# Optimization experiments

Measured on AMD Instinct MI355X. Metric: run time of the kernel, lower is better.

## Reference

```python
import jax, jax.numpy as jnp
import numpy as np

N, E, D, H = 50000, 800000, 64, 8
DH = D // H
EPS = 1e-5


def _bn(x, gamma, beta):
    # BatchNorm1d in training mode: biased variance over the node axis
    m = x.mean(axis=0)
    v = ((x - m) ** 2).mean(axis=0)
    return (x - m) * jax.lax.rsqrt(v + EPS) * gamma + beta


def setup_inputs() -> dict:
    key = jax.random.key(0)
    ks = jax.random.split(key, 12)
    s_in = 1.0 / np.sqrt(D)
    s_ff = 1.0 / np.sqrt(2 * D)
    inp = {
        "h": jax.random.normal(ks[0], (N, D), dtype=jnp.float32),
        "src": jax.random.randint(ks[1], (E,), 0, N, dtype=jnp.int32),
        "dst": jax.random.randint(ks[2], (E,), 0, N, dtype=jnp.int32),
        "Wq": jax.random.normal(ks[3], (D, D), dtype=jnp.float32) * s_in,
        "bq": jnp.zeros((D,), jnp.float32),
        "Wk": jax.random.normal(ks[4], (D, D), dtype=jnp.float32) * s_in,
        "bk": jnp.zeros((D,), jnp.float32),
        "Wv": jax.random.normal(ks[5], (D, D), dtype=jnp.float32) * s_in,
        "bv": jnp.zeros((D,), jnp.float32),
        "g1": jnp.ones((D,), jnp.float32),
        "b1": jnp.zeros((D,), jnp.float32),
        "W1": jax.random.normal(ks[6], (D, 2 * D), dtype=jnp.float32) * s_in,
        "bb1": jnp.zeros((2 * D,), jnp.float32),
        "W2": jax.random.normal(ks[7], (2 * D, D), dtype=jnp.float32) * s_ff,
        "bb2": jnp.zeros((D,), jnp.float32),
        "g2": jnp.ones((D,), jnp.float32),
        "b2": jnp.zeros((D,), jnp.float32),
    }
    return inp


def reference(h, src, dst, Wq, bq, Wk, bk, Wv, bv, g1, b1, W1, bb1, W2, bb2, g2, b2):
    scale = np.sqrt(DH).astype(np.float32)
    Q = (h @ Wq + bq).reshape(N, H, DH)
    K = (h @ Wk + bk).reshape(N, H, DH)
    V = (h @ Wv + bv).reshape(N, H, DH)

    # per-edge score: K[src] . Q[dst], clamped/scaled exp  -> [E, H]
    score = jnp.sum(K[src] * Q[dst], axis=-1)
    score = jnp.exp(jnp.clip(score / scale, -5.0, 5.0))

    # weighted-value and normalizer scatter-sums onto dst nodes
    wV = jax.ops.segment_sum(V[src] * score[:, :, None], dst, num_segments=N)  # [N,H,DH]
    z = jax.ops.segment_sum(score, dst, num_segments=N)  # [N,H]

    safe_z = jnp.where(z == 0, 1.0, z)
    head = jnp.where((z == 0)[:, :, None], 0.0, wV / safe_z[:, :, None])  # nan -> 0
    attn = head.reshape(N, D)

    h1 = _bn(h + attn, g1, b1)
    ffn = jax.nn.relu(h1 @ W1 + bb1) @ W2 + bb2
    out = _bn(h1 + ffn, g2, b2)
    return out
```

## Files before the change

### kernel.cpp

```cpp
#include <hip/hip_runtime.h>
#include <hip/hip_fp16.h>
#include <math.h>

#define N_NODES 50000
#define E_EDGES 800000
#define EPS_BN  1e-5f
#define INV_N   (1.0f / N_NODES)
#define SCAN_BLOCKS 196
#define QKV_BLOCKS  782
#define HIST_BLOCKS 3125

__global__ __launch_bounds__(256) void qkv_hist_kernel(
    const float* __restrict__ h,
    const float* __restrict__ Wq, const float* __restrict__ bq,
    const float* __restrict__ Wk, const float* __restrict__ bk,
    const float* __restrict__ Wv, const float* __restrict__ bv,
    float* __restrict__ Q, __half* __restrict__ KV,
    const int* __restrict__ dst, int* __restrict__ count)
{
    __shared__ float  xs[64][68];
    __shared__ __half Wqh[64][64];
    __shared__ __half Wkh[64][64];
    __shared__ __half Wvh[64][64];
    const int t = threadIdx.x;

    if (blockIdx.x >= QKV_BLOCKS) {
        const int e = (blockIdx.x - QKV_BLOCKS) * 256 + t;
        if (e < E_EDGES) atomicAdd(&count[dst[e]], 1);
        return;
    }

    const int tx = t & 15;
    const int ty = t >> 4;
    const int row0 = blockIdx.x * 64;

    {
        __half2* wq = (__half2*)&Wqh[0][0];
        __half2* wk = (__half2*)&Wkh[0][0];
        __half2* wv = (__half2*)&Wvh[0][0];
        #pragma unroll
        for (int k = 0; k < 4; ++k) {
            const int i = t + k * 256;
            const float4 a = *(const float4*)(Wq + i * 4);
            wq[i * 2]     = __floats2half2_rn(a.x, a.y);
            wq[i * 2 + 1] = __floats2half2_rn(a.z, a.w);
            const float4 b = *(const float4*)(Wk + i * 4);
            wk[i * 2]     = __floats2half2_rn(b.x, b.y);
            wk[i * 2 + 1] = __floats2half2_rn(b.z, b.w);
            const float4 c = *(const float4*)(Wv + i * 4);
            wv[i * 2]     = __floats2half2_rn(c.x, c.y);
            wv[i * 2 + 1] = __floats2half2_rn(c.z, c.w);
        }
    }

    #pragma unroll
    for (int k = 0; k < 4; ++k) {
        const int i  = t + k * 256;
        const int r  = i >> 4;
        const int c4 = (i & 15) * 4;
        float4 v = make_float4(0.f, 0.f, 0.f, 0.f);
        if (row0 + r < N_NODES)
            v = *(const float4*)(h + (size_t)(row0 + r) * 64 + c4);
        *(float4*)(&xs[r][c4]) = v;
    }
    __syncthreads();

    const int c0 = tx * 4;
    float4 aq[4], ak[4], av[4];
    const float4 bq4 = *(const float4*)(bq + c0);
    const float4 bk4 = *(const float4*)(bk + c0);
    const float4 bv4 = *(const float4*)(bv + c0);
    #pragma unroll
    for (int i = 0; i < 4; ++i) { aq[i] = bq4; ak[i] = bk4; av[i] = bv4; }

    #pragma unroll 4
    for (int c = 0; c < 64; ++c) {
        const __half2* qp = (const __half2*)&Wqh[c][c0];
        const __half2* kp = (const __half2*)&Wkh[c][c0];
        const __half2* vp = (const __half2*)&Wvh[c][c0];
        const float2 wq0 = __half22float2(qp[0]);
        const float2 wq1 = __half22float2(qp[1]);
        const float2 wk0 = __half22float2(kp[0]);
        const float2 wk1 = __half22float2(kp[1]);
        const float2 wv0 = __half22float2(vp[0]);
        const float2 wv1 = __half22float2(vp[1]);
        #pragma unroll
        for (int i = 0; i < 4; ++i) {
            const float xv = xs[ty * 4 + i][c];
            aq[i].x = fmaf(xv, wq0.x, aq[i].x); aq[i].y = fmaf(xv, wq0.y, aq[i].y);
            aq[i].z = fmaf(xv, wq1.x, aq[i].z); aq[i].w = fmaf(xv, wq1.y, aq[i].w);
            ak[i].x = fmaf(xv, wk0.x, ak[i].x); ak[i].y = fmaf(xv, wk0.y, ak[i].y);
            ak[i].z = fmaf(xv, wk1.x, ak[i].z); ak[i].w = fmaf(xv, wk1.y, ak[i].w);
            av[i].x = fmaf(xv, wv0.x, av[i].x); av[i].y = fmaf(xv, wv0.y, av[i].y);
            av[i].z = fmaf(xv, wv1.x, av[i].z); av[i].w = fmaf(xv, wv1.y, av[i].w);
        }
    }
    #pragma unroll
    for (int i = 0; i < 4; ++i) {
        const int row = row0 + ty * 4 + i;
        if (row < N_NODES) {
            *(float4*)(Q + (size_t)row * 64 + c0) = aq[i];
            __half* kvp = KV + ((size_t)(c0 >> 3) * N_NODES + row) * 16 + (c0 & 7);
            *(__half2*)(kvp)         = __floats2half2_rn(ak[i].x, ak[i].y);
            *(__half2*)(kvp + 2)     = __floats2half2_rn(ak[i].z, ak[i].w);
            *(__half2*)(kvp + 8)     = __floats2half2_rn(av[i].x, av[i].y);
            *(__half2*)(kvp + 8 + 2) = __floats2half2_rn(av[i].z, av[i].w);
        }
    }
}

__global__ __launch_bounds__(256) void scanA_kernel(
    const int* __restrict__ count,
    int* __restrict__ rowStart, int* __restrict__ blockSums)
{
    __shared__ int ls[256];
    const int t = threadIdx.x;
    const int i = blockIdx.x * 256 + t;
    const int v = (i < N_NODES) ? count[i] : 0;
    ls[t] = v;
    __syncthreads();
    #pragma unroll
    for (int off = 1; off < 256; off <<= 1) {
        const int u = (t >= off) ? ls[t - off] : 0;
        __syncthreads();
        ls[t] += u;
        __syncthreads();
    }
    if (i < N_NODES) rowStart[i] = ls[t] - v;
    if (t == 255) blockSums[blockIdx.x] = ls[255];
}

__global__ __launch_bounds__(256) void scanBC_kernel(
    int* __restrict__ rowStart, int* __restrict__ cursor,
    const int* __restrict__ blockSums)
{
    __shared__ int ls[256];
    const int t = threadIdx.x;
    const int v = (t < SCAN_BLOCKS) ? blockSums[t] : 0;
    ls[t] = v;
    __syncthreads();
    #pragma unroll
    for (int off = 1; off < 256; off <<= 1) {
        const int u = (t >= off) ? ls[t - off] : 0;
        __syncthreads();
        ls[t] += u;
        __syncthreads();
    }
    const int exc = ls[t] - v;
    __syncthreads();
    ls[t] = exc;
    __syncthreads();
    const int boff = ls[blockIdx.x];
    const int i = blockIdx.x * 256 + t;
    if (i < N_NODES) {
        const int r = rowStart[i] + boff;
        rowStart[i] = r;
        cursor[i]   = r;
    }
    if (i == 0) rowStart[N_NODES] = E_EDGES;
}

__global__ __launch_bounds__(256) void scatter_kernel(
    const int* __restrict__ src, const int* __restrict__ dst,
    int* __restrict__ cursor, unsigned short* __restrict__ srcSorted)
{
    const int e0 = blockIdx.x * 512 + threadIdx.x;
    const int e1 = e0 + 256;
    const bool h0 = e0 < E_EDGES;
    const bool h1 = e1 < E_EDGES;
    const int s0 = h0 ? src[e0] : 0;
    const int d0 = h0 ? dst[e0] : 0;
    const int s1 = h1 ? src[e1] : 0;
    const int d1 = h1 ? dst[e1] : 0;
    if (h0) srcSorted[atomicAdd(&cursor[d0], 1)] = (unsigned short)s0;
    if (h1) srcSorted[atomicAdd(&cursor[d1], 1)] = (unsigned short)s1;
}

__global__ __launch_bounds__(256) void gather_edge_kernel(
    const float* __restrict__ h,
    const float* __restrict__ Q, const __half* __restrict__ KV,
    const int* __restrict__ rowStart, const unsigned short* __restrict__ srcSorted,
    float* __restrict__ x, float* __restrict__ s1, float* __restrict__ sq1)
{
    const int lane = threadIdx.x & 63;
    const int wave = threadIdx.x >> 6;
    const int slot = lane & 7;
    const int ns   = lane >> 3;
    const int hh   = blockIdx.x & 7;
    const int chunk0  = blockIdx.x >> 3;
    const int nChunks = gridDim.x >> 3;
    const __half* __restrict__ KVh = KV + (size_t)hh * N_NODES * 16;

    float bsum[8], bsq[8];
    #pragma unroll
    for (int j = 0; j < 8; ++j) { bsum[j] = 0.0f; bsq[j] = 0.0f; }

    for (int chunk = chunk0; chunk * 32 < N_NODES; chunk += nChunks) {
        const int n = chunk * 32 + wave * 8 + ns;
        const bool valid = (n < N_NODES);
        int start = 0, end = 0;
        float4 q0 = make_float4(0.f, 0.f, 0.f, 0.f), q1 = q0;
        if (valid) {
            start = rowStart[n];
            end   = rowStart[n + 1];
            q0 = *(const float4*)(Q + (size_t)n * 64 + hh * 8);
            q1 = *(const float4*)(Q + (size_t)n * 64 + hh * 8 + 4);
        }
        float a0=0,a1=0,a2=0,a3=0,a4=0,a5=0,a6=0,a7=0,zacc=0;
        for (int e = start + slot; e < end; e += 16) {
            const int s0 = srcSorted[e];
            const int e1 = e + 8;
            const bool has1 = (e1 < end);
            const int s1i = has1 ? (int)srcSorted[e1] : s0;
            const __half* kv0 = KVh + (size_t)s0 * 16;
            const __half* kv1 = KVh + (size_t)s1i * 16;
            const float4 kraw0 = *(const float4*)(kv0);
            const float4 vraw0 = *(const float4*)(kv0 + 8);
            const float4 kraw1 = *(const float4*)(kv1);
            const float4 vraw1 = *(const float4*)(kv1 + 8);

            {
                const __half2* kh = (const __half2*)&kraw0;
                const float2 ka = __half22float2(kh[0]);
                const float2 kb = __half22float2(kh[1]);
                const float2 kc = __half22float2(kh[2]);
                const float2 kd = __half22float2(kh[3]);
                float sc = ka.x*q0.x + ka.y*q0.y + kb.x*q0.z + kb.y*q0.w
                         + kc.x*q1.x + kc.y*q1.y + kd.x*q1.z + kd.y*q1.w;
                sc *= 0.35355339059327373f;
                sc = fminf(5.0f, fmaxf(-5.0f, sc));
                const float p = __expf(sc);
                const __half2* vh = (const __half2*)&vraw0;
                const float2 va = __half22float2(vh[0]);
                const float2 vb = __half22float2(vh[1]);
                const float2 vc = __half22float2(vh[2]);
                const float2 vd = __half22float2(vh[3]);
                a0 = fmaf(p, va.x, a0); a1 = fmaf(p, va.y, a1);
                a2 = fmaf(p, vb.x, a2); a3 = fmaf(p, vb.y, a3);
                a4 = fmaf(p, vc.x, a4); a5 = fmaf(p, vc.y, a5);
                a6 = fmaf(p, vd.x, a6); a7 = fmaf(p, vd.y, a7);
                zacc += p;
            }
            if (has1) {
                const __half2* kh = (const __half2*)&kraw1;
                const float2 ka = __half22float2(kh[0]);
                const float2 kb = __half22float2(kh[1]);
                const float2 kc = __half22float2(kh[2]);
                const float2 kd = __half22float2(kh[3]);
                float sc = ka.x*q0.x + ka.y*q0.y + kb.x*q0.z + kb.y*q0.w
                         + kc.x*q1.x + kc.y*q1.y + kd.x*q1.z + kd.y*q1.w;
                sc *= 0.35355339059327373f;
                sc = fminf(5.0f, fmaxf(-5.0f, sc));
                const float p = __expf(sc);
                const __half2* vh = (const __half2*)&vraw1;
                const float2 va = __half22float2(vh[0]);
                const float2 vb = __half22float2(vh[1]);
                const float2 vc = __half22float2(vh[2]);
                const float2 vd = __half22float2(vh[3]);
                a0 = fmaf(p, va.x, a0); a1 = fmaf(p, va.y, a1);
                a2 = fmaf(p, vb.x, a2); a3 = fmaf(p, vb.y, a3);
                a4 = fmaf(p, vc.x, a4); a5 = fmaf(p, vc.y, a5);
                a6 = fmaf(p, vd.x, a6); a7 = fmaf(p, vd.y, a7);
                zacc += p;
            }
        }
        #pragma unroll
        for (int m = 1; m < 8; m <<= 1) {
            a0 += __shfl_xor(a0, m, 64); a1 += __shfl_xor(a1, m, 64);
            a2 += __shfl_xor(a2, m, 64); a3 += __shfl_xor(a3, m, 64);
            a4 += __shfl_xor(a4, m, 64); a5 += __shfl_xor(a5, m, 64);
            a6 += __shfl_xor(a6, m, 64); a7 += __shfl_xor(a7, m, 64);
            zacc += __shfl_xor(zacc, m, 64);
        }
        if (slot == 0 && valid) {
            const float inv = (zacc == 0.0f) ? 0.0f : 1.0f / zacc;
            const float4 h0 = *(const float4*)(h + (size_t)n * 64 + hh * 8);
            const float4 h1 = *(const float4*)(h + (size_t)n * 64 + hh * 8 + 4);
            float xv[8];
            xv[0] = fmaf(a0, inv, h0.x); xv[1] = fmaf(a1, inv, h0.y);
            xv[2] = fmaf(a2, inv, h0.z); xv[3] = fmaf(a3, inv, h0.w);
            xv[4] = fmaf(a4, inv, h1.x); xv[5] = fmaf(a5, inv, h1.y);
            xv[6] = fmaf(a6, inv, h1.z); xv[7] = fmaf(a7, inv, h1.w);
            *(float4*)(x + (size_t)n * 64 + hh * 8)     =
                make_float4(xv[0], xv[1], xv[2], xv[3]);
            *(float4*)(x + (size_t)n * 64 + hh * 8 + 4) =
                make_float4(xv[4], xv[5], xv[6], xv[7]);
            #pragma unroll
            for (int j = 0; j < 8; ++j) {
                bsum[j] += xv[j];
                bsq[j]  += xv[j] * xv[j];
            }
        }
    }
    __shared__ float lsm[32][8];
    __shared__ float lsq[32][8];
    if (slot == 0) {
        #pragma unroll
        for (int j = 0; j < 8; ++j) {
            lsm[wave * 8 + ns][j] = bsum[j];
            lsq[wave * 8 + ns][j] = bsq[j];
        }
    }
    __syncthreads();
    if (threadIdx.x < 8) {
        const int tt = threadIdx.x;
        float ss = 0.f, qq = 0.f;
        #pragma unroll
        for (int k = 0; k < 32; ++k) { ss += lsm[k][tt]; qq += lsq[k][tt]; }
        atomicAdd(s1 + hh * 8 + tt, ss);
        atomicAdd(sq1 + hh * 8 + tt, qq);
    }
}

__global__ __launch_bounds__(512, 4) void ffn_kernel(
    const float* __restrict__ x,
    const float* __restrict__ s1, const float* __restrict__ sq1,
    const float* __restrict__ g1, const float* __restrict__ b1,
    const float* __restrict__ W1, const float* __restrict__ bb1,
    const float* __restrict__ W2, const float* __restrict__ bb2,
    float* __restrict__ y, float* __restrict__ s2, float* __restrict__ sq2)
{
    __shared__ __half W1h[64][128];
    __shared__ __half W2h[128][64];
    __shared__ float  xs[64][64];
    __shared__ __half ts[64][128];

    const int t  = threadIdx.x;
    const int tx = t & 15;
    const int ty = t >> 4;
    const int row0 = blockIdx.x * 64;

    {
        __half2* w1p = (__half2*)&W1h[0][0];
        __half2* w2p = (__half2*)&W2h[0][0];
        #pragma unroll
        for (int k = 0; k < 4; ++k) {
            const int i = t + k * 512;
            const float4 w1 = *(const float4*)(W1 + i * 4);
            w1p[i * 2]     = __floats2half2_rn(w1.x, w1.y);
            w1p[i * 2 + 1] = __floats2half2_rn(w1.z, w1.w);
            const float4 w2 = *(const float4*)(W2 + i * 4);
            w2p[i * 2]     = __floats2half2_rn(w2.x, w2.y);
            w2p[i * 2 + 1] = __floats2half2_rn(w2.z, w2.w);
        }
    }

    {
        const int c4 = tx * 4;
        const float4 ssum = *(const float4*)(s1 + c4);
        const float4 sqs  = *(const float4*)(sq1 + c4);
        const float4 gg   = *(const float4*)(g1 + c4);
        const float4 bb   = *(const float4*)(b1 + c4);
        float4 mm, rr, A, C;
        mm.x = ssum.x * INV_N; mm.y = ssum.y * INV_N;
        mm.z = ssum.z * INV_N; mm.w = ssum.w * INV_N;
        rr.x = rsqrtf(sqs.x * INV_N - mm.x * mm.x + EPS_BN);
        rr.y = rsqrtf(sqs.y * INV_N - mm.y * mm.y + EPS_BN);
        rr.z = rsqrtf(sqs.z * INV_N - mm.z * mm.z + EPS_BN);
        rr.w = rsqrtf(sqs.w * INV_N - mm.w * mm.w + EPS_BN);
        A.x = rr.x * gg.x; C.x = bb.x - mm.x * A.x;
        A.y = rr.y * gg.y; C.y = bb.y - mm.y * A.y;
        A.z = rr.z * gg.z; C.z = bb.z - mm.z * A.z;
        A.w = rr.w * gg.w; C.w = bb.w - mm.w * A.w;
        #pragma unroll
        for (int k = 0; k < 2; ++k) {
            const int i = t + k * 512;
            const int r = i >> 4;
            float4 v = make_float4(0.f, 0.f, 0.f, 0.f);
            if (row0 + r < N_NODES) {
                const float4 xv = *(const float4*)(x + (size_t)(row0 + r) * 64 + c4);
                v.x = fmaf(xv.x, A.x, C.x);
                v.y = fmaf(xv.y, A.y, C.y);
                v.z = fmaf(xv.z, A.z, C.z);
                v.w = fmaf(xv.w, A.w, C.w);
            }
            *(float4*)(&xs[r][c4]) = v;
        }
    }
    __syncthreads();

    const int r0 = ty * 2, r1 = r0 + 1;

    {
        const int cA = tx * 4, cB = 64 + tx * 4;
        float4 aA0 = make_float4(0,0,0,0), aA1 = aA0, aB0 = aA0, aB1 = aA0;
        #pragma unroll 4
        for (int c = 0; c < 64; ++c) {
            const __half2* wAp = (const __half2*)&W1h[c][cA];
            const __half2* wBp = (const __half2*)&W1h[c][cB];
            const float2 wa0 = __half22float2(wAp[0]);
            const float2 wa1 = __half22float2(wAp[1]);
            const float2 wb0 = __half22float2(wBp[0]);
            const float2 wb1 = __half22float2(wBp[1]);
            const float x0 = xs[r0][c];
            const float x1 = xs[r1][c];
            aA0.x = fmaf(x0, wa0.x, aA0.x); aA0.y = fmaf(x0, wa0.y, aA0.y);
            aA0.z = fmaf(x0, wa1.x, aA0.z); aA0.w = fmaf(x0, wa1.y, aA0.w);
            aA1.x = fmaf(x1, wa0.x, aA1.x); aA1.y = fmaf(x1, wa0.y, aA1.y);
            aA1.z = fmaf(x1, wa1.x, aA1.z); aA1.w = fmaf(x1, wa1.y, aA1.w);
            aB0.x = fmaf(x0, wb0.x, aB0.x); aB0.y = fmaf(x0, wb0.y, aB0.y);
            aB0.z = fmaf(x0, wb1.x, aB0.z); aB0.w = fmaf(x0, wb1.y, aB0.w);
            aB1.x = fmaf(x1, wb0.x, aB1.x); aB1.y = fmaf(x1, wb0.y, aB1.y);
            aB1.z = fmaf(x1, wb1.x, aB1.z); aB1.w = fmaf(x1, wb1.y, aB1.w);
        }
        const float4 b1A = *(const float4*)(bb1 + cA);
        const float4 b1B = *(const float4*)(bb1 + cB);
        aA0.x = fmaxf(aA0.x + b1A.x, 0.f); aA0.y = fmaxf(aA0.y + b1A.y, 0.f);
        aA0.z = fmaxf(aA0.z + b1A.z, 0.f); aA0.w = fmaxf(aA0.w + b1A.w, 0.f);
        aA1.x = fmaxf(aA1.x + b1A.x, 0.f); aA1.y = fmaxf(aA1.y + b1A.y, 0.f);
        aA1.z = fmaxf(aA1.z + b1A.z, 0.f); aA1.w = fmaxf(aA1.w + b1A.w, 0.f);
        aB0.x = fmaxf(aB0.x + b1B.x, 0.f); aB0.y = fmaxf(aB0.y + b1B.y, 0.f);
        aB0.z = fmaxf(aB0.z + b1B.z, 0.f); aB0.w = fmaxf(aB0.w + b1B.w, 0.f);
        aB1.x = fmaxf(aB1.x + b1B.x, 0.f); aB1.y = fmaxf(aB1.y + b1B.y, 0.f);
        aB1.z = fmaxf(aB1.z + b1B.z, 0.f); aB1.w = fmaxf(aB1.w + b1B.w, 0.f);
        *(__half2*)&ts[r0][cA]     = __floats2half2_rn(aA0.x, aA0.y);
        *(__half2*)&ts[r0][cA + 2] = __floats2half2_rn(aA0.z, aA0.w);
        *(__half2*)&ts[r1][cA]     = __floats2half2_rn(aA1.x, aA1.y);
        *(__half2*)&ts[r1][cA + 2] = __floats2half2_rn(aA1.z, aA1.w);
        *(__half2*)&ts[r0][cB]     = __floats2half2_rn(aB0.x, aB0.y);
        *(__half2*)&ts[r0][cB + 2] = __floats2half2_rn(aB0.z, aB0.w);
        *(__half2*)&ts[r1][cB]     = __floats2half2_rn(aB1.x, aB1.y);
        *(__half2*)&ts[r1][cB + 2] = __floats2half2_rn(aB1.z, aB1.w);
    }
    __syncthreads();

    float4 s = make_float4(0,0,0,0), q = s;
    {
        const int c4 = tx * 4;
        float4 y0 = make_float4(0,0,0,0), y1 = y0;
        #pragma unroll 4
        for (int k = 0; k < 128; ++k) {
            const __half2* wp = (const __half2*)&W2h[k][c4];
            const float2 wa = __half22float2(wp[0]);
            const float2 wb = __half22float2(wp[1]);
            const float T0 = __half2float(ts[r0][k]);
            const float T1 = __half2float(ts[r1][k]);
            y0.x = fmaf(T0, wa.x, y0.x); y0.y = fmaf(T0, wa.y, y0.y);
            y0.z = fmaf(T0, wb.x, y0.z); y0.w = fmaf(T0, wb.y, y0.w);
            y1.x = fmaf(T1, wa.x, y1.x); y1.y = fmaf(T1, wa.y, y1.y);
            y1.z = fmaf(T1, wb.x, y1.z); y1.w = fmaf(T1, wb.y, y1.w);
        }
        const float4 bb = *(const float4*)(bb2 + c4);
        const float4 h0 = *(const float4*)(&xs[r0][c4]);
        const float4 h1v = *(const float4*)(&xs[r1][c4]);
        y0.x += bb.x + h0.x;  y0.y += bb.y + h0.y;
        y0.z += bb.z + h0.z;  y0.w += bb.w + h0.w;
        y1.x += bb.x + h1v.x; y1.y += bb.y + h1v.y;
        y1.z += bb.z + h1v.z; y1.w += bb.w + h1v.w;

        const bool v0 = (row0 + r0) < N_NODES;
        const bool v1 = (row0 + r1) < N_NODES;
        if (v0) *(float4*)(y + (size_t)(row0 + r0) * 64 + c4) = y0;
        if (v1) *(float4*)(y + (size_t)(row0 + r1) * 64 + c4) = y1;

        if (v0) {
            s.x += y0.x; s.y += y0.y; s.z += y0.z; s.w += y0.w;
            q.x += y0.x*y0.x; q.y += y0.y*y0.y; q.z += y0.z*y0.z; q.w += y0.w*y0.w;
        }
        if (v1) {
            s.x += y1.x; s.y += y1.y; s.z += y1.z; s.w += y1.w;
            q.x += y1.x*y1.x; q.y += y1.y*y1.y; q.z += y1.z*y1.z; q.w += y1.w*y1.w;
        }
    }
    {
        float* red = (float*)&W1h[0][0];
        const int c4 = tx * 4;
        *(float4*)(red + ty * 64 + c4)        = s;
        *(float4*)(red + (32 + ty) * 64 + c4) = q;
    }
    __syncthreads();
    if (t < 64) {
        const float* red = (const float*)&W1h[0][0];
        float ss = 0.f, qq = 0.f;
        #pragma unroll
        for (int k = 0; k < 32; ++k) {
            ss += red[k * 64 + t];
            qq += red[(32 + k) * 64 + t];
        }
        atomicAdd(s2 + t, ss);
        atomicAdd(sq2 + t, qq);
    }
}

__global__ __launch_bounds__(256) void bn2_apply_kernel(
    float* __restrict__ y,
    const float* __restrict__ s2, const float* __restrict__ sq2,
    const float* __restrict__ g2, const float* __restrict__ b2)
{
    const int c4 = (threadIdx.x & 15) * 4;
    const float4 ssum = *(const float4*)(s2 + c4);
    const float4 sqs  = *(const float4*)(sq2 + c4);
    const float4 gg   = *(const float4*)(g2 + c4);
    const float4 bb   = *(const float4*)(b2 + c4);
    float4 mm, rr, A, C;
    mm.x = ssum.x * INV_N; mm.y = ssum.y * INV_N;
    mm.z = ssum.z * INV_N; mm.w = ssum.w * INV_N;
    rr.x = rsqrtf(sqs.x * INV_N - mm.x * mm.x + EPS_BN);
    rr.y = rsqrtf(sqs.y * INV_N - mm.y * mm.y + EPS_BN);
    rr.z = rsqrtf(sqs.z * INV_N - mm.z * mm.z + EPS_BN);
    rr.w = rsqrtf(sqs.w * INV_N - mm.w * mm.w + EPS_BN);
    A.x = rr.x * gg.x; C.x = bb.x - mm.x * A.x;
    A.y = rr.y * gg.y; C.y = bb.y - mm.y * A.y;
    A.z = rr.z * gg.z; C.z = bb.z - mm.z * A.z;
    A.w = rr.w * gg.w; C.w = bb.w - mm.w * A.w;

    const int total4 = N_NODES * 16;
    const int stride = gridDim.x * blockDim.x;
    for (int i = blockIdx.x * blockDim.x + threadIdx.x; i < total4; i += stride) {
        float4 v = *((float4*)y + i);
        v.x = fmaf(v.x, A.x, C.x);
        v.y = fmaf(v.y, A.y, C.y);
        v.z = fmaf(v.z, A.z, C.z);
        v.w = fmaf(v.w, A.w, C.w);
        *((float4*)y + i) = v;
    }
}

extern "C" void kernel_launch(void* const* d_in, const int* in_sizes, int n_in,
                              void* d_out, int out_size, void* d_ws, size_t ws_size,
                              hipStream_t stream)
{
    const float* h   = (const float*)d_in[0];
    const int*   src = (const int*)d_in[1];
    const int*   dst = (const int*)d_in[2];
    const float* Wq  = (const float*)d_in[3];
    const float* bq  = (const float*)d_in[4];
    const float* Wk  = (const float*)d_in[5];
    const float* bk  = (const float*)d_in[6];
    const float* Wv  = (const float*)d_in[7];
    const float* bv  = (const float*)d_in[8];
    const float* g1  = (const float*)d_in[9];
    const float* b1  = (const float*)d_in[10];
    const float* W1  = (const float*)d_in[11];
    const float* bb1 = (const float*)d_in[12];
    const float* W2  = (const float*)d_in[13];
    const float* bb2 = (const float*)d_in[14];
    const float* g2  = (const float*)d_in[15];
    const float* b2  = (const float*)d_in[16];
    float* out = (float*)d_out;

    float* ws = (float*)d_ws;
    const size_t ND = (size_t)N_NODES * 64;
    float* Q  = ws;
    __half* KV = (__half*)(ws + ND);
    float* x  = Q;
    unsigned short* srcSorted = (unsigned short*)(ws + 3 * ND);
    int* count     = (int*)(srcSorted + E_EDGES);
    float* st      = (float*)(count + N_NODES);
    int* rowStart  = (int*)(st + 512);
    int* cursor    = rowStart + N_NODES + 1;
    int* blockSums = cursor + N_NODES;
    float* s1 = st,       *sq1 = st + 64;
    float* s2 = st + 256, *sq2 = st + 320;

    hipMemsetAsync(count, 0, (N_NODES + 512) * sizeof(int), stream);

    qkv_hist_kernel<<<QKV_BLOCKS + HIST_BLOCKS, 256, 0, stream>>>(
        h, Wq, bq, Wk, bk, Wv, bv, Q, KV, dst, count);
    scanA_kernel<<<SCAN_BLOCKS, 256, 0, stream>>>(count, rowStart, blockSums);
    scanBC_kernel<<<SCAN_BLOCKS, 256, 0, stream>>>(rowStart, cursor, blockSums);
    scatter_kernel<<<(E_EDGES + 511) / 512, 256, 0, stream>>>(
        src, dst, cursor, srcSorted);
    gather_edge_kernel<<<1024, 256, 0, stream>>>(h, Q, KV, rowStart, srcSorted,
                                                 x, s1, sq1);
    ffn_kernel<<<(N_NODES + 63) / 64, 512, 0, stream>>>(
        x, s1, sq1, g1, b1, W1, bb1, W2, bb2, out, s2, sq2);
    bn2_apply_kernel<<<2048, 256, 0, stream>>>(out, s2, sq2, g2, b2);
}
```

Baseline: 293.3 us.

## Store Q and h head-major and unroll edge gather four-deep

The QKV kernel now writes Q and a copy of h in head-major [H][N][8] layout, so each per-head gather block reads contiguous 32-byte rows instead of strided slices of 64-wide rows. The edge loop is unrolled from two to four edges per slot so more independent KV loads are in flight per lane. In exchange the QKV kernel writes an extra N×D buffer, the workspace grows, and x no longer aliases Q.

```diff
diff --git a/kernel.cpp b/kernel.cpp
--- a/kernel.cpp
+++ b/kernel.cpp
@@ -15,7 +15,7 @@
     const float* __restrict__ Wq, const float* __restrict__ bq,
     const float* __restrict__ Wk, const float* __restrict__ bk,
     const float* __restrict__ Wv, const float* __restrict__ bv,
-    float* __restrict__ Q, __half* __restrict__ KV,
+    float* __restrict__ Qh, float* __restrict__ hpart, __half* __restrict__ KV,
     const int* __restrict__ dst, int* __restrict__ count)
 {
     __shared__ float  xs[64][68];
@@ -95,12 +95,16 @@
             av[i].z = fmaf(xv, wv1.x, av[i].z); av[i].w = fmaf(xv, wv1.y, av[i].w);
         }
     }
+    const int head = c0 >> 3;
+    const int off  = c0 & 7;
     #pragma unroll
     for (int i = 0; i < 4; ++i) {
         const int row = row0 + ty * 4 + i;
         if (row < N_NODES) {
-            *(float4*)(Q + (size_t)row * 64 + c0) = aq[i];
-            __half* kvp = KV + ((size_t)(c0 >> 3) * N_NODES + row) * 16 + (c0 & 7);
+            const size_t nb8 = ((size_t)head * N_NODES + row) * 8 + off;
+            *(float4*)(Qh + nb8)    = aq[i];
+            *(float4*)(hpart + nb8) = *(const float4*)(&xs[ty * 4 + i][c0]);
+            __half* kvp = KV + ((size_t)head * N_NODES + row) * 16 + off;
             *(__half2*)(kvp)         = __floats2half2_rn(ak[i].x, ak[i].y);
             *(__half2*)(kvp + 2)     = __floats2half2_rn(ak[i].z, ak[i].w);
             *(__half2*)(kvp + 8)     = __floats2half2_rn(av[i].x, av[i].y);
@@ -177,8 +181,8 @@
 }
 
 __global__ __launch_bounds__(256) void gather_edge_kernel(
-    const float* __restrict__ h,
-    const float* __restrict__ Q, const __half* __restrict__ KV,
+    const float* __restrict__ Qh, const float* __restrict__ hpart,
+    const __half* __restrict__ KV,
     const int* __restrict__ rowStart, const unsigned short* __restrict__ srcSorted,
     float* __restrict__ x, float* __restrict__ s1, float* __restrict__ sq1)
 {
@@ -190,6 +194,8 @@
     const int chunk0  = blockIdx.x >> 3;
     const int nChunks = gridDim.x >> 3;
     const __half* __restrict__ KVh = KV + (size_t)hh * N_NODES * 16;
+    const float*  __restrict__ Qhh = Qh + (size_t)hh * N_NODES * 8;
+    const float*  __restrict__ hph = hpart + (size_t)hh * N_NODES * 8;
 
     float bsum[8], bsq[8];
     #pragma unroll
@@ -203,67 +209,62 @@
         if (valid) {
             start = rowStart[n];
             end   = rowStart[n + 1];
-            q0 = *(const float4*)(Q + (size_t)n * 64 + hh * 8);
-            q1 = *(const float4*)(Q + (size_t)n * 64 + hh * 8 + 4);
+            q0 = *(const float4*)(Qhh + (size_t)n * 8);
+            q1 = *(const float4*)(Qhh + (size_t)n * 8 + 4);
         }
         float a0=0,a1=0,a2=0,a3=0,a4=0,a5=0,a6=0,a7=0,zacc=0;
-        for (int e = start + slot; e < end; e += 16) {
+
+#define GE_PROC(kraw, vraw)                                                  \
+        {                                                                    \
+            const __half2* kh = (const __half2*)&(kraw);                     \
+            const float2 ka = __half22float2(kh[0]);                         \
+            const float2 kb = __half22float2(kh[1]);                         \
+            const float2 kc = __half22float2(kh[2]);                         \
+            const float2 kd = __half22float2(kh[3]);                         \
+            float sc = ka.x*q0.x + ka.y*q0.y + kb.x*q0.z + kb.y*q0.w         \
+                     + kc.x*q1.x + kc.y*q1.y + kd.x*q1.z + kd.y*q1.w;        \
+            sc *= 0.35355339059327373f;                                      \
+            sc = fminf(5.0f, fmaxf(-5.0f, sc));                              \
+            const float p = __expf(sc);                                      \
+            const __half2* vh = (const __half2*)&(vraw);                     \
+            const float2 va = __half22float2(vh[0]);                         \
+            const float2 vb = __half22float2(vh[1]);                         \
+            const float2 vc = __half22float2(vh[2]);                         \
+            const float2 vd = __half22float2(vh[3]);                         \
+            a0 = fmaf(p, va.x, a0); a1 = fmaf(p, va.y, a1);                  \
+            a2 = fmaf(p, vb.x, a2); a3 = fmaf(p, vb.y, a3);                  \
+            a4 = fmaf(p, vc.x, a4); a5 = fmaf(p, vc.y, a5);                  \
+            a6 = fmaf(p, vd.x, a6); a7 = fmaf(p, vd.y, a7);                  \
+            zacc += p;                                                       \
+        }
+
+        for (int e = start + slot; e < end; e += 32) {
+            const int e1i = e + 8, e2i = e + 16, e3i = e + 24;
+            const bool b1 = e1i < end, b2 = e2i < end, b3 = e3i < end;
             const int s0 = srcSorted[e];
-            const int e1 = e + 8;
-            const bool has1 = (e1 < end);
-            const int s1i = has1 ? (int)srcSorted[e1] : s0;
-            const __half* kv0 = KVh + (size_t)s0 * 16;
-            const __half* kv1 = KVh + (size_t)s1i * 16;
-            const float4 kraw0 = *(const float4*)(kv0);
-            const float4 vraw0 = *(const float4*)(kv0 + 8);
-            const float4 kraw1 = *(const float4*)(kv1);
-            const float4 vraw1 = *(const float4*)(kv1 + 8);
-
-            {
-                const __half2* kh = (const __half2*)&kraw0;
-                const float2 ka = __half22float2(kh[0]);
-                const float2 kb = __half22float2(kh[1]);
-                const float2 kc = __half22float2(kh[2]);
-                const float2 kd = __half22float2(kh[3]);
-                float sc = ka.x*q0.x + ka.y*q0.y + kb.x*q0.z + kb.y*q0.w
-                         + kc.x*q1.x + kc.y*q1.y + kd.x*q1.z + kd.y*q1.w;
-                sc *= 0.35355339059327373f;
-                sc = fminf(5.0f, fmaxf(-5.0f, sc));
-                const float p = __expf(sc);
-                const __half2* vh = (const __half2*)&vraw0;
-                const float2 va = __half22float2(vh[0]);
-                const float2 vb = __half22float2(vh[1]);
-                const float2 vc = __half22float2(vh[2]);
-                const float2 vd = __half22float2(vh[3]);
-                a0 = fmaf(p, va.x, a0); a1 = fmaf(p, va.y, a1);
-                a2 = fmaf(p, vb.x, a2); a3 = fmaf(p, vb.y, a3);
-                a4 = fmaf(p, vc.x, a4); a5 = fmaf(p, vc.y, a5);
-                a6 = fmaf(p, vd.x, a6); a7 = fmaf(p, vd.y, a7);
-                zacc += p;
-            }
-            if (has1) {
-                const __half2* kh = (const __half2*)&kraw1;
-                const float2 ka = __half22float2(kh[0]);
-                const float2 kb = __half22float2(kh[1]);
-                const float2 kc = __half22float2(kh[2]);
-                const float2 kd = __half22float2(kh[3]);
-                float sc = ka.x*q0.x + ka.y*q0.y + kb.x*q0.z + kb.y*q0.w
-                         + kc.x*q1.x + kc.y*q1.y + kd.x*q1.z + kd.y*q1.w;
-                sc *= 0.35355339059327373f;
-                sc = fminf(5.0f, fmaxf(-5.0f, sc));
-                const float p = __expf(sc);
-                const __half2* vh = (const __half2*)&vraw1;
-                const float2 va = __half22float2(vh[0]);
-                const float2 vb = __half22float2(vh[1]);
-                const float2 vc = __half22float2(vh[2]);
-                const float2 vd = __half22float2(vh[3]);
-                a0 = fmaf(p, va.x, a0); a1 = fmaf(p, va.y, a1);
-                a2 = fmaf(p, vb.x, a2); a3 = fmaf(p, vb.y, a3);
-                a4 = fmaf(p, vc.x, a4); a5 = fmaf(p, vc.y, a5);
-                a6 = fmaf(p, vd.x, a6); a7 = fmaf(p, vd.y, a7);
-                zacc += p;
-            }
-        }
+            const int s1i = b1 ? (int)srcSorted[e1i] : s0;
+            const int s2i = b2 ? (int)srcSorted[e2i] : s0;
+            const int s3i = b3 ? (int)srcSorted[e3i] : s0;
+            const __half* p0 = KVh + (size_t)s0 * 16;
+            const __half* p1 = KVh + (size_t)s1i * 16;
+            const __half* p2 = KVh + (size_t)s2i * 16;
+            const __half* p3 = KVh + (size_t)s3i * 16;
+            const float4 k0 = *(const float4*)(p0);
+            const float4 v0 = *(const float4*)(p0 + 8);
+            const float4 k1 = *(const float4*)(p1);
+            const float4 v1 = *(const float4*)(p1 + 8);
+            const float4 k2 = *(const float4*)(p2);
+            const float4 v2 = *(const float4*)(p2 + 8);
+            const float4 k3 = *(const float4*)(p3);
+            const float4 v3 = *(const float4*)(p3 + 8);
+
+            GE_PROC(k0, v0);
+            if (b1) GE_PROC(k1, v1);
+            if (b2) GE_PROC(k2, v2);
+            if (b3) GE_PROC(k3, v3);
+        }
+#undef GE_PROC
+
         #pragma unroll
         for (int m = 1; m < 8; m <<= 1) {
             a0 += __shfl_xor(a0, m, 64); a1 += __shfl_xor(a1, m, 64);
@@ -274,8 +275,8 @@
         }
         if (slot == 0 && valid) {
             const float inv = (zacc == 0.0f) ? 0.0f : 1.0f / zacc;
-            const float4 h0 = *(const float4*)(h + (size_t)n * 64 + hh * 8);
-            const float4 h1 = *(const float4*)(h + (size_t)n * 64 + hh * 8 + 4);
+            const float4 h0 = *(const float4*)(hph + (size_t)n * 8);
+            const float4 h1 = *(const float4*)(hph + (size_t)n * 8 + 4);
             float xv[8];
             xv[0] = fmaf(a0, inv, h0.x); xv[1] = fmaf(a1, inv, h0.y);
             xv[2] = fmaf(a2, inv, h0.z); xv[3] = fmaf(a3, inv, h0.w);
@@ -541,10 +542,11 @@
 
     float* ws = (float*)d_ws;
     const size_t ND = (size_t)N_NODES * 64;
-    float* Q  = ws;
-    __half* KV = (__half*)(ws + ND);
-    float* x  = Q;
-    unsigned short* srcSorted = (unsigned short*)(ws + 3 * ND);
+    float* Qh    = ws;
+    float* hpart = ws + ND;
+    __half* KV   = (__half*)(ws + 2 * ND);
+    float* x     = ws + 3 * ND;
+    unsigned short* srcSorted = (unsigned short*)(ws + 4 * ND);
     int* count     = (int*)(srcSorted + E_EDGES);
     float* st      = (float*)(count + N_NODES);
     int* rowStart  = (int*)(st + 512);
@@ -556,13 +558,13 @@
     hipMemsetAsync(count, 0, (N_NODES + 512) * sizeof(int), stream);
 
     qkv_hist_kernel<<<QKV_BLOCKS + HIST_BLOCKS, 256, 0, stream>>>(
-        h, Wq, bq, Wk, bk, Wv, bv, Q, KV, dst, count);
+        h, Wq, bq, Wk, bk, Wv, bv, Qh, hpart, KV, dst, count);
     scanA_kernel<<<SCAN_BLOCKS, 256, 0, stream>>>(count, rowStart, blockSums);
     scanBC_kernel<<<SCAN_BLOCKS, 256, 0, stream>>>(rowStart, cursor, blockSums);
     scatter_kernel<<<(E_EDGES + 511) / 512, 256, 0, stream>>>(
         src, dst, cursor, srcSorted);
-    gather_edge_kernel<<<1024, 256, 0, stream>>>(h, Q, KV, rowStart, srcSorted,
-                                                 x, s1, sq1);
+    gather_edge_kernel<<<1024, 256, 0, stream>>>(Qh, hpart, KV, rowStart,
+                                                 srcSorted, x, s1, sq1);
     ffn_kernel<<<(N_NODES + 63) / 64, 512, 0, stream>>>(
         x, s1, sq1, g1, b1, W1, bb1, W2, bb2, out, s2, sq2);
     bn2_apply_kernel<<<2048, 256, 0, stream>>>(out, s2, sq2, g2, b2);
```

New measurement: 306.9 us. 4.6% more time.
